# Kernel optimization log

Hardware: AMD Instinct MI355X
Metric: run time of the kernel (lower is better)

## Reference

```python
import jax, jax.numpy as jnp
import numpy as np

B, N_P, N_S = 64, 50, 200
N_NODES = N_P * N_S          # 10000 nodes per graph (jobs x ops)
N_CAND = N_S + 1             # 201 candidates
INPUT_DIM, HIDDEN = 3, 64
NODE_DIM = 2 * HIDDEN        # h_nodes feature dim (=> actor in = 6*HIDDEN)
POOL_DIM = 4 * HIDDEN        # h_pooled dim (mean || max pooling)
H_ACTOR, H_CRITIC = 256, 256


def setup_inputs() -> dict:
    key = jax.random.key(0)
    ks = jax.random.split(key, 16)
    p = lambda k, sh: jax.random.normal(k, sh, jnp.float32) * 0.02
    x = jax.random.normal(ks[0], (B, N_NODES, INPUT_DIM), jnp.float32)
    candidate = jax.random.randint(ks[1], (B, N_CAND), 0, N_NODES)
    mask = jax.random.randint(ks[2], (B, N_CAND), 0, 2) > 0
    mask = mask.at[:, 0].set(True)  # guarantee at least one valid action per row
    return {
        "x": x, "candidate": candidate, "mask": mask,
        "fe_w1": p(ks[3], (INPUT_DIM, HIDDEN)), "fe_b1": jnp.zeros((HIDDEN,), jnp.float32),
        "fe_w2": p(ks[4], (HIDDEN, NODE_DIM)), "fe_b2": jnp.zeros((NODE_DIM,), jnp.float32),
        "a_w1": p(ks[5], (NODE_DIM + POOL_DIM, H_ACTOR)), "a_b1": jnp.zeros((H_ACTOR,), jnp.float32),
        "a_w2": p(ks[6], (H_ACTOR, H_ACTOR)), "a_b2": jnp.zeros((H_ACTOR,), jnp.float32),
        "a_w3": p(ks[7], (H_ACTOR, 1)), "a_b3": jnp.zeros((1,), jnp.float32),
        "c_w1": p(ks[8], (POOL_DIM, H_CRITIC)), "c_b1": jnp.zeros((H_CRITIC,), jnp.float32),
        "c_w2": p(ks[9], (H_CRITIC, H_CRITIC)), "c_b2": jnp.zeros((H_CRITIC,), jnp.float32),
        "c_w3": p(ks[10], (H_CRITIC, 1)), "c_b3": jnp.zeros((1,), jnp.float32),
    }


def _actor_critic(x, candidate, mask,
                  fe_w1, fe_b1, fe_w2, fe_b2,
                  a_w1, a_b1, a_w2, a_b2, a_w3, a_b3,
                  c_w1, c_b1, c_w2, c_b2, c_w3, c_b3):
    # --- feature_extract: per-node MLP embedding, graph-level pooling ---
    h = jax.nn.relu(jnp.einsum('bni,ih->bnh', x, fe_w1) + fe_b1)
    h_nodes = jax.nn.relu(jnp.einsum('bnh,hd->bnd', h, fe_w2) + fe_b2)   # [B, N, 2H]
    h_pooled = jnp.concatenate([h_nodes.mean(axis=1), h_nodes.max(axis=1)], axis=-1)  # [B, 4H]

    # --- gather candidate node features (torch.gather over node axis) ---
    cand_feat = jnp.take_along_axis(h_nodes, candidate[:, :, None], axis=1)  # [B, C, 2H]

    # --- concat broadcast pooled feature ---
    pooled_rep = jnp.broadcast_to(h_pooled[:, None, :], (cand_feat.shape[0], cand_feat.shape[1], h_pooled.shape[-1]))
    concat_fea = jnp.concatenate([cand_feat, pooled_rep], axis=-1)  # [B, C, 6H]

    # --- actor MLP (tanh hidden layers, linear out) ---
    a = jnp.tanh(concat_fea @ a_w1 + a_b1)
    a = jnp.tanh(a @ a_w2 + a_b2)
    scores = a @ a_w3 + a_b3                                    # [B, C, 1]

    # --- mask with -inf, softmax over candidate axis ---
    scores = jnp.where(mask[:, :, None], scores, -jnp.inf)
    pi = jax.nn.softmax(scores, axis=1)                          # [B, C, 1]

    # --- critic MLP on pooled feature ---
    c = jnp.tanh(h_pooled @ c_w1 + c_b1)
    c = jnp.tanh(c @ c_w2 + c_b2)
    v = c @ c_w3 + c_b3                                          # [B, 1]
    return pi, v


def reference(x, candidate, mask,
              fe_w1, fe_b1, fe_w2, fe_b2,
              a_w1, a_b1, a_w2, a_b2, a_w3, a_b3,
              c_w1, c_b1, c_w2, c_b2, c_w3, c_b3):
    return _actor_critic(x, candidate, mask,
                         fe_w1, fe_b1, fe_w2, fe_b2,
                         a_w1, a_b1, a_w2, a_b2, a_w3, a_b3,
                         c_w1, c_b1, c_w2, c_b2, c_w3, c_b3)
```

## Files before the change

### kernel.cpp

```cpp
#include <hip/hip_runtime.h>

#define NN 10000
#define NCAND 201
#define NB 64

typedef __attribute__((ext_vector_type(8))) short short8;
typedef __attribute__((ext_vector_type(4))) float f32x4;

__device__ __forceinline__ float bf2f(unsigned short u) {
  return __uint_as_float(((unsigned int)u) << 16);
}
__device__ __forceinline__ unsigned short f2bf(float f) {
  unsigned int u = __float_as_uint(f);
  u += 0x7FFFu + ((u >> 16) & 1u);
  return (unsigned short)(u >> 16);
}
__device__ __forceinline__ float fast_tanh(float x) {
  return 1.0f - 2.0f / (__expf(2.0f * x) + 1.0f);
}
__device__ __forceinline__ float gld(const void* p, long i, int f) {
  return f ? ((const float*)p)[i] : bf2f(((const unsigned short*)p)[i]);
}

__global__ __launch_bounds__(256)
void detect_kernel(const void* x, const void* w1, const void* b1, const void* w2,
                   const void* b2, const void* aw1, const void* ab1, const void* aw2,
                   const void* ab2, const void* aw3, const void* ab3,
                   const void* cw1, const void* cb1, const void* cw2, const void* cb2,
                   const void* cw3, const void* cb3,
                   const unsigned int* mask_w, const unsigned int* cand_w,
                   int* F, float* zero_base) {
  const void* ptrs[17] = {x, w1, b1, w2, b2, aw1, ab1, aw2, ab2, aw3, ab3,
                          cw1, cb1, cw2, cb2, cw3, cb3};
  const int sizes[17] = {1920000, 192, 64, 8192, 128, 98304, 256, 65536, 256,
                         256, 1, 65536, 256, 65536, 256, 256, 1};
  const int t = threadIdx.x;
  const int j = blockIdx.x;
  __shared__ int sh[3];
  if (t < 3) sh[t] = 0;
  __syncthreads();
  if (j < 17) {
    const unsigned short* p = (const unsigned short*)ptrs[j];
    int K = min(sizes[j], 2048);
    int c = 0;
    for (int i = t; i < K; i += 256)
      if ((p[i] & 0x7F80u) >= 0x4300u) c++;
    if (c) atomicAdd(&sh[0], c);
    __syncthreads();
    if (t == 0) F[j] = (sh[0] > (K >> 3)) ? 1 : 0;
  } else if (j == 17) {
    int flo = 0, fhi = 0, fgt = 0;
    for (int i = t; i < 3216; i += 256) {
      unsigned int w = mask_w[i];
      if ((w & 0xFFFFu) == 0x3F80u) flo = 1;
      if ((w >> 16) == 0x3F80u) fhi = 1;
      if (w > 1u) fgt = 1;
    }
    if (flo) sh[0] = 1;
    if (fhi) sh[1] = 1;
    if (fgt) sh[2] = 1;
    __syncthreads();
    if (t == 0) F[17] = sh[0] ? 2 : (sh[1] ? 3 : (sh[2] ? 1 : 0));
  } else if (j == 18) {
    int co = 0;
    for (int i = t; i < 1024; i += 256)
      if ((i & 1) && cand_w[i] != 0u) co = 1;
    if (co) sh[0] = 1;
    __syncthreads();
    if (t == 0) F[18] = sh[0] ? 0 : 1;
  } else {
    zero_base[(j - 19) * 256 + t] = 0.f;
  }
}

__global__ __launch_bounds__(256)
void prep_kernel(const void* __restrict__ fe_w2, const void* __restrict__ a_w1,
                 const void* __restrict__ a_w2,
                 const void* __restrict__ c_w1, const void* __restrict__ c_w2,
                 const int* __restrict__ F,
                 unsigned short* __restrict__ w2t, unsigned short* __restrict__ aw1t,
                 unsigned short* __restrict__ aw2t,
                 unsigned short* __restrict__ cw1t, unsigned short* __restrict__ cw2t) {
  const int F3 = F[3], F5 = F[5], F7 = F[7], F11 = F[11], F13 = F[13];
  int i = blockIdx.x * 256 + threadIdx.x;
  if (i < 128 * 64) { int n = i >> 6, k = i & 63; w2t[i] = f2bf(gld(fe_w2, k * 128 + n, F3)); }
  if (i < 256 * 384) { int n = i / 384, k = i % 384; aw1t[i] = f2bf(gld(a_w1, k * 256 + n, F5)); }
  if (i < 256 * 256) {
    int n = i >> 8, k = i & 255;
    aw2t[i] = f2bf(gld(a_w2, k * 256 + n, F7));
    cw1t[i] = f2bf(gld(c_w1, k * 256 + n, F11));
    cw2t[i] = f2bf(gld(c_w2, k * 256 + n, F13));
  }
}

__global__ __launch_bounds__(256, 4)
void feat_pool_kernel(const void* __restrict__ x,
                      const void* __restrict__ w1, const void* __restrict__ b1,
                      const unsigned short* __restrict__ w2t,
                      const void* __restrict__ b2,
                      const int* __restrict__ F,
                      float* __restrict__ psum, float* __restrict__ pmax) {
  __shared__ __align__(16) unsigned short h1s[128 * 72];
  __shared__ float w1f[3 * 64];
  __shared__ float b1f[64];
  __shared__ float b2f[128];

  const int t = threadIdx.x;
  const int b = blockIdx.x >> 4;
  const int s = blockIdx.x & 15;
  const int lane = t & 63;
  const int wv = t >> 6;
  const int F0 = F[0], F1 = F[1], F2 = F[2], F4 = F[4];

  if (t < 192) w1f[t] = gld(w1, t, F1);
  if (t < 64) b1f[t] = gld(b1, t, F2);
  if (t < 128) b2f[t] = gld(b2, t, F4);

  short8 bfr[2][2];
#pragma unroll
  for (int nl = 0; nl < 2; ++nl)
#pragma unroll
    for (int ks = 0; ks < 2; ++ks) {
      int col = wv * 32 + nl * 16 + (lane & 15);
      bfr[nl][ks] = *(const short8*)(w2t + col * 64 + ((lane >> 4) * 8) + ks * 32);
    }
  __syncthreads();

  float csum[2] = {0.f, 0.f};
  float cmax[2] = {0.f, 0.f};

  const int m = t & 127;
  const int kg = t >> 7;

  float x0 = 0.f, x1 = 0.f, x2 = 0.f;
  {
    int c0 = s;
    if (c0 < 79) {
      int nb = c0 * 128;
      if (m < min(128, NN - nb)) {
        long xo = ((long)b * NN + nb + m) * 3;
        x0 = gld(x, xo, F0); x1 = gld(x, xo + 1, F0); x2 = gld(x, xo + 2, F0);
      }
    }
  }

  for (int c = s; c < 79; c += 16) {
    int nb = c * 128;
    int cnt = (nb + 128 <= NN) ? 128 : (NN - nb);
    if (m < cnt) {
#pragma unroll
      for (int blk = 0; blk < 4; ++blk) {
        short8 v;
#pragma unroll
        for (int i = 0; i < 8; ++i) {
          int k = kg * 32 + blk * 8 + i;
          float vv = x0 * w1f[k] + x1 * w1f[64 + k] + x2 * w1f[128 + k] + b1f[k];
          v[i] = (short)f2bf(fmaxf(vv, 0.f));
        }
        *(short8*)(h1s + m * 72 + kg * 32 + blk * 8) = v;
      }
    }
    {
      int cn = c + 16;
      float nx0 = 0.f, nx1 = 0.f, nx2 = 0.f;
      if (cn < 79) {
        int nbn = cn * 128;
        if (m < min(128, NN - nbn)) {
          long xo = ((long)b * NN + nbn + m) * 3;
          nx0 = gld(x, xo, F0); nx1 = gld(x, xo + 1, F0); nx2 = gld(x, xo + 2, F0);
        }
      }
      __syncthreads();
      x0 = nx0; x1 = nx1; x2 = nx2;
    }
#pragma unroll
    for (int mt = 0; mt < 8; ++mt) {
      const unsigned short* ap = h1s + (mt * 16 + (lane & 15)) * 72 + ((lane >> 4) * 8);
      short8 af0 = *(const short8*)(ap);
      short8 af1 = *(const short8*)(ap + 32);
#pragma unroll
      for (int nl = 0; nl < 2; ++nl) {
        f32x4 acc = {0.f, 0.f, 0.f, 0.f};
        acc = __builtin_amdgcn_mfma_f32_16x16x32_bf16(af0, bfr[nl][0], acc, 0, 0, 0);
        acc = __builtin_amdgcn_mfma_f32_16x16x32_bf16(af1, bfr[nl][1], acc, 0, 0, 0);
        int col = wv * 32 + nl * 16 + (lane & 15);
        float bb = b2f[col];
#pragma unroll
        for (int r = 0; r < 4; ++r) {
          int row = mt * 16 + ((lane >> 4) * 4) + r;
          if (row < cnt) {
            float v = fmaxf(acc[r] + bb, 0.f);
            csum[nl] += v;
            cmax[nl] = fmaxf(cmax[nl], v);
          }
        }
      }
    }
    __syncthreads();
  }
#pragma unroll
  for (int nl = 0; nl < 2; ++nl) {
    csum[nl] += __shfl_xor(csum[nl], 16);
    csum[nl] += __shfl_xor(csum[nl], 32);
    cmax[nl] = fmaxf(cmax[nl], __shfl_xor(cmax[nl], 16));
    cmax[nl] = fmaxf(cmax[nl], __shfl_xor(cmax[nl], 32));
  }
  if (lane < 16) {
#pragma unroll
    for (int nl = 0; nl < 2; ++nl) {
      int col = wv * 32 + nl * 16 + lane;
      atomicAdd(&psum[b * 128 + col], csum[nl]);
      atomicMax((int*)&pmax[b * 128 + col], __float_as_int(cmax[nl]));
    }
  }
}

__global__ __launch_bounds__(256)
void actor_kernel(const void* __restrict__ x, const int* __restrict__ cand,
                  const void* __restrict__ w1, const void* __restrict__ b1,
                  const void* __restrict__ b2bf,
                  const void* __restrict__ ab1, const void* __restrict__ ab2,
                  const void* __restrict__ aw3, const void* __restrict__ ab3,
                  const int* __restrict__ F,
                  const float* __restrict__ psum, const float* __restrict__ pmax,
                  const unsigned short* __restrict__ w2t,
                  const unsigned short* __restrict__ aw1t,
                  const unsigned short* __restrict__ aw2t,
                  float* __restrict__ scores) {
  __shared__ __align__(16) unsigned short h1c[32 * 72];
  __shared__ __align__(16) unsigned short cf[32 * 136];
  __shared__ __align__(16) unsigned short a1s[32 * 264];
  __shared__ __align__(16) unsigned short a2s[32 * 264];
  __shared__ __align__(16) unsigned short plbf[256];
  __shared__ float ab1f[256], ab2f[256], b2f[128];

  const int t = threadIdx.x;
  const int b = blockIdx.x / 7;
  const int cb = blockIdx.x % 7;
  const int cbase = cb * 29;
  const int cntc = min(29, NCAND - cbase);
  const int lane = t & 63;
  const int wv = t >> 6;
  const int F0 = F[0], F1 = F[1], F2 = F[2], F4 = F[4], F6 = F[6], F8 = F[8];
  const int F9 = F[9], F10 = F[10], C64 = F[18];

  if (t < 128) {
    plbf[t] = f2bf(psum[b * 128 + t] * (1.0f / 10000.0f));
    plbf[128 + t] = f2bf(pmax[b * 128 + t]);
    b2f[t] = gld(b2bf, t, F4);
  }
  ab1f[t] = gld(ab1, t, F6);
  ab2f[t] = gld(ab2, t, F8);

  {
    int r = t & 31;
    int ci = cbase + r;
    if (ci > NCAND - 1) ci = NCAND - 1;
    long cidx = (long)b * NCAND + ci;
    int nd = C64 ? cand[2 * cidx] : cand[cidx];
    long xo = ((long)b * NN + nd) * 3;
    float x0 = gld(x, xo, F0), x1 = gld(x, xo + 1, F0), x2 = gld(x, xo + 2, F0);
    int kg = t >> 5;
#pragma unroll
    for (int i = 0; i < 8; ++i) {
      int k = kg * 8 + i;
      float v = x0 * gld(w1, k, F1) + x1 * gld(w1, 64 + k, F1) +
                x2 * gld(w1, 128 + k, F1) + gld(b1, k, F2);
      h1c[r * 72 + k] = f2bf(fmaxf(v, 0.f));
    }
  }
  __syncthreads();

  {
    short8 af[2][2];
#pragma unroll
    for (int mt = 0; mt < 2; ++mt)
#pragma unroll
      for (int ks = 0; ks < 2; ++ks)
        af[mt][ks] = *(const short8*)(h1c + (mt * 16 + (lane & 15)) * 72 + ((lane >> 4) * 8) + ks * 32);
#pragma unroll
    for (int nl = 0; nl < 2; ++nl) {
      int col = wv * 32 + nl * 16 + (lane & 15);
      short8 bf0 = *(const short8*)(w2t + col * 64 + ((lane >> 4) * 8));
      short8 bf1 = *(const short8*)(w2t + col * 64 + ((lane >> 4) * 8) + 32);
      float bb = b2f[col];
#pragma unroll
      for (int mt = 0; mt < 2; ++mt) {
        f32x4 acc = {0.f, 0.f, 0.f, 0.f};
        acc = __builtin_amdgcn_mfma_f32_16x16x32_bf16(af[mt][0], bf0, acc, 0, 0, 0);
        acc = __builtin_amdgcn_mfma_f32_16x16x32_bf16(af[mt][1], bf1, acc, 0, 0, 0);
#pragma unroll
        for (int r = 0; r < 4; ++r) {
          int row = mt * 16 + ((lane >> 4) * 4) + r;
          cf[row * 136 + col] = f2bf(fmaxf(acc[r] + bb, 0.f));
        }
      }
    }
  }
  __syncthreads();

  {
    f32x4 acc[2][4];
#pragma unroll
    for (int mt = 0; mt < 2; ++mt)
#pragma unroll
      for (int nt = 0; nt < 4; ++nt) acc[mt][nt] = (f32x4){0.f, 0.f, 0.f, 0.f};
    for (int ks = 0; ks < 12; ++ks) {
      short8 af0, af1;
      if (ks < 4) {
        af0 = *(const short8*)(cf + (lane & 15) * 136 + ks * 32 + ((lane >> 4) * 8));
        af1 = *(const short8*)(cf + (16 + (lane & 15)) * 136 + ks * 32 + ((lane >> 4) * 8));
      } else {
        short8 p = *(const short8*)(plbf + (ks - 4) * 32 + ((lane >> 4) * 8));
        af0 = p;
        af1 = p;
      }
#pragma unroll
      for (int nt = 0; nt < 4; ++nt) {
        int col = wv * 64 + nt * 16 + (lane & 15);
        short8 bfr = *(const short8*)(aw1t + col * 384 + ks * 32 + ((lane >> 4) * 8));
        acc[0][nt] = __builtin_amdgcn_mfma_f32_16x16x32_bf16(af0, bfr, acc[0][nt], 0, 0, 0);
        acc[1][nt] = __builtin_amdgcn_mfma_f32_16x16x32_bf16(af1, bfr, acc[1][nt], 0, 0, 0);
      }
    }
#pragma unroll
    for (int mt = 0; mt < 2; ++mt)
#pragma unroll
      for (int nt = 0; nt < 4; ++nt) {
        int col = wv * 64 + nt * 16 + (lane & 15);
        float bb = ab1f[col];
#pragma unroll
        for (int r = 0; r < 4; ++r) {
          int row = mt * 16 + ((lane >> 4) * 4) + r;
          a1s[row * 264 + col] = f2bf(fast_tanh(acc[mt][nt][r] + bb));
        }
      }
  }
  __syncthreads();

  {
    f32x4 acc[2][4];
#pragma unroll
    for (int mt = 0; mt < 2; ++mt)
#pragma unroll
      for (int nt = 0; nt < 4; ++nt) acc[mt][nt] = (f32x4){0.f, 0.f, 0.f, 0.f};
    for (int ks = 0; ks < 8; ++ks) {
      short8 af0 = *(const short8*)(a1s + (lane & 15) * 264 + ks * 32 + ((lane >> 4) * 8));
      short8 af1 = *(const short8*)(a1s + (16 + (lane & 15)) * 264 + ks * 32 + ((lane >> 4) * 8));
#pragma unroll
      for (int nt = 0; nt < 4; ++nt) {
        int col = wv * 64 + nt * 16 + (lane & 15);
        short8 bfr = *(const short8*)(aw2t + col * 256 + ks * 32 + ((lane >> 4) * 8));
        acc[0][nt] = __builtin_amdgcn_mfma_f32_16x16x32_bf16(af0, bfr, acc[0][nt], 0, 0, 0);
        acc[1][nt] = __builtin_amdgcn_mfma_f32_16x16x32_bf16(af1, bfr, acc[1][nt], 0, 0, 0);
      }
    }
#pragma unroll
    for (int mt = 0; mt < 2; ++mt)
#pragma unroll
      for (int nt = 0; nt < 4; ++nt) {
        int col = wv * 64 + nt * 16 + (lane & 15);
        float bb = ab2f[col];
#pragma unroll
        for (int r = 0; r < 4; ++r) {
          int row = mt * 16 + ((lane >> 4) * 4) + r;
          a2s[row * 264 + col] = f2bf(fast_tanh(acc[mt][nt][r] + bb));
        }
      }
  }
  __syncthreads();

  {
    int row = t >> 3, seg = t & 7;
    float p = 0.f;
#pragma unroll 8
    for (int i = 0; i < 32; ++i) {
      int k = seg * 32 + i;
      p += bf2f(a2s[row * 264 + k]) * gld(aw3, k, F9);
    }
    p += __shfl_xor(p, 1);
    p += __shfl_xor(p, 2);
    p += __shfl_xor(p, 4);
    if (seg == 0 && row < cntc)
      scores[b * 256 + cbase + row] = p + gld(ab3, 0, F10);
  }
}

__global__ __launch_bounds__(256)
void softmax_critic_kernel(const float* __restrict__ scores,
                           const void* __restrict__ mask,
                           const int* __restrict__ F,
                           const float* __restrict__ psum,
                           const float* __restrict__ pmax,
                           const unsigned short* __restrict__ cw1t,
                           const unsigned short* __restrict__ cw2t,
                           const void* __restrict__ cb1, const void* __restrict__ cb2,
                           const void* __restrict__ cw3, const void* __restrict__ cb3,
                           void* __restrict__ out) {
  __shared__ float plf[256];
  __shared__ float c1f[256];
  __shared__ float red[4];
  const int t = threadIdx.x, b = blockIdx.x;
  const int lane = t & 63, wv = t >> 6;
  const int MM = F[17];
  const int OF = (F[0] + F[1] + F[3] + F[5] + F[7] + F[9] + F[11] + F[13] + F[15]) >= 5;
  const int F12 = F[12], F14 = F[14], F15 = F[15], F16 = F[16];

  if (t < 128) {
    plf[t] = psum[b * 128 + t] * (1.0f / 10000.0f);
    plf[128 + t] = pmax[b * 128 + t];
  }

  float sraw = 0.f, sv = -1e30f;
  bool valid = false;
  if (t < NCAND) {
    sraw = scores[b * 256 + t];
    long idx = (long)b * NCAND + t;
    if (MM == 0)      valid = ((const int*)mask)[idx] != 0;
    else if (MM == 1) valid = ((const unsigned char*)mask)[idx] != 0;
    else if (MM == 2) valid = ((const unsigned short*)mask)[idx] != 0;
    else              valid = ((const unsigned int*)mask)[idx] != 0;
    if (valid) sv = sraw;
  }
  float m = sv;
  for (int o = 32; o; o >>= 1) m = fmaxf(m, __shfl_xor(m, o));
  if (lane == 0) red[wv] = m;
  __syncthreads();
  m = fmaxf(fmaxf(red[0], red[1]), fmaxf(red[2], red[3]));
  __syncthreads();
  float e = valid ? __expf(sraw - m) : 0.f;
  if (!(e == e)) e = 0.f;
  float ss = e;
  for (int o = 32; o; o >>= 1) ss += __shfl_xor(ss, o);
  if (lane == 0) red[wv] = ss;
  __syncthreads();
  float tot = red[0] + red[1] + red[2] + red[3];
  tot = fmaxf(tot, 1e-30f);
  if (t < NCAND) {
    float pv = e / tot;
    if (!(pv == pv)) pv = 0.f;
    if (OF) ((float*)out)[b * NCAND + t] = pv;
    else ((unsigned short*)out)[b * NCAND + t] = f2bf(pv);
  }
  __syncthreads();

  {
    float a = gld(cb1, t, F12);
    const unsigned short* row = cw1t + t * 256;
#pragma unroll
    for (int k8 = 0; k8 < 32; ++k8) {
      short8 w = *(const short8*)(row + k8 * 8);
#pragma unroll
      for (int j = 0; j < 8; ++j)
        a += plf[k8 * 8 + j] * bf2f((unsigned short)w[j]);
    }
    c1f[t] = fast_tanh(a);
  }
  __syncthreads();
  {
    float a2 = gld(cb2, t, F14);
    const unsigned short* row = cw2t + t * 256;
#pragma unroll
    for (int k8 = 0; k8 < 32; ++k8) {
      short8 w = *(const short8*)(row + k8 * 8);
#pragma unroll
      for (int j = 0; j < 8; ++j)
        a2 += c1f[k8 * 8 + j] * bf2f((unsigned short)w[j]);
    }
    a2 = fast_tanh(a2);
    float p = a2 * gld(cw3, t, F15);
    for (int o = 32; o; o >>= 1) p += __shfl_xor(p, o);
    __syncthreads();
    if (lane == 0) red[wv] = p;
    __syncthreads();
    if (t == 0) {
      float v = red[0] + red[1] + red[2] + red[3] + gld(cb3, 0, F16);
      if (!(v == v)) v = 0.f;
      if (OF) ((float*)out)[NB * NCAND + b] = v;
      else ((unsigned short*)out)[NB * NCAND + b] = f2bf(v);
    }
  }
}

extern "C" void kernel_launch(void* const* d_in, const int* in_sizes, int n_in,
                              void* d_out, int out_size, void* d_ws, size_t ws_size,
                              hipStream_t stream) {
  const void* x = d_in[0];
  const int* cand = (const int*)d_in[1];
  const void* mask = d_in[2];
  const void* fe_w1 = d_in[3];
  const void* fe_b1 = d_in[4];
  const void* fe_w2 = d_in[5];
  const void* fe_b2 = d_in[6];
  const void* a_w1 = d_in[7];
  const void* a_b1 = d_in[8];
  const void* a_w2 = d_in[9];
  const void* a_b2 = d_in[10];
  const void* a_w3 = d_in[11];
  const void* a_b3 = d_in[12];
  const void* c_w1 = d_in[13];
  const void* c_b1 = d_in[14];
  const void* c_w2 = d_in[15];
  const void* c_b2 = d_in[16];
  const void* c_w3 = d_in[17];
  const void* c_b3 = d_in[18];

  char* ws = (char*)d_ws;
  float* psum = (float*)(ws + 0);
  float* pmax = (float*)(ws + 32768);
  float* scores = (float*)(ws + 65536);
  unsigned short* w2t = (unsigned short*)(ws + 131072);
  unsigned short* aw1t = (unsigned short*)(ws + 147456);
  unsigned short* aw2t = (unsigned short*)(ws + 344064);
  int* F = (int*)(ws + 475136);
  unsigned short* cw1t = (unsigned short*)(ws + 475264);
  unsigned short* cw2t = (unsigned short*)(ws + 606336);

  detect_kernel<<<83, 256, 0, stream>>>(x, fe_w1, fe_b1, fe_w2, fe_b2,
                                        a_w1, a_b1, a_w2, a_b2, a_w3, a_b3,
                                        c_w1, c_b1, c_w2, c_b2, c_w3, c_b3,
                                        (const unsigned int*)mask,
                                        (const unsigned int*)cand, F, psum);
  prep_kernel<<<384, 256, 0, stream>>>(fe_w2, a_w1, a_w2, c_w1, c_w2, F,
                                       w2t, aw1t, aw2t, cw1t, cw2t);
  feat_pool_kernel<<<1024, 256, 0, stream>>>(x, fe_w1, fe_b1, w2t, fe_b2, F, psum, pmax);
  actor_kernel<<<448, 256, 0, stream>>>(x, cand, fe_w1, fe_b1, fe_b2,
                                        a_b1, a_b2, a_w3, a_b3, F, psum, pmax,
                                        w2t, aw1t, aw2t, scores);
  softmax_critic_kernel<<<64, 256, 0, stream>>>(scores, mask, F, psum, pmax,
                                                cw1t, cw2t, c_b1, c_b2, c_w3, c_b3,
                                                (void*)d_out);
}
```

Baseline: 171.3 us.

## Merge dtype detection into weight prep kernel and split softmax/critic blocks

Merges the detect and weight-transpose kernels into a single launch. Each prep block now recomputes the dtype flags for the five transposed weights locally, counting over the first 2048 elements in shared memory, so it no longer has to wait for a separate detect kernel. The softmax/critic kernel moves from 64 to 128 blocks: the first 64 do the masked softmax and the other 64 run the critic MLP, so both run in parallel. This removes one launch and serialisation point, at the cost of each prep block rereading 10K sample elements.

```diff
diff --git a/kernel.cpp b/kernel.cpp
--- a/kernel.cpp
+++ b/kernel.cpp
@@ -23,32 +23,66 @@
 }
 
 __global__ __launch_bounds__(256)
-void detect_kernel(const void* x, const void* w1, const void* b1, const void* w2,
-                   const void* b2, const void* aw1, const void* ab1, const void* aw2,
-                   const void* ab2, const void* aw3, const void* ab3,
-                   const void* cw1, const void* cb1, const void* cw2, const void* cb2,
-                   const void* cw3, const void* cb3,
-                   const unsigned int* mask_w, const unsigned int* cand_w,
-                   int* F, float* zero_base) {
-  const void* ptrs[17] = {x, w1, b1, w2, b2, aw1, ab1, aw2, ab2, aw3, ab3,
-                          cw1, cb1, cw2, cb2, cw3, cb3};
-  const int sizes[17] = {1920000, 192, 64, 8192, 128, 98304, 256, 65536, 256,
-                         256, 1, 65536, 256, 65536, 256, 256, 1};
+void prep_kernel(const void* x, const void* w1, const void* b1, const void* w2,
+                 const void* b2, const void* aw1, const void* ab1, const void* aw2,
+                 const void* ab2, const void* aw3, const void* ab3,
+                 const void* cw1, const void* cb1, const void* cw2, const void* cb2,
+                 const void* cw3, const void* cb3,
+                 const unsigned int* mask_w, const unsigned int* cand_w,
+                 int* F, float* zero_base,
+                 unsigned short* __restrict__ w2t, unsigned short* __restrict__ aw1t,
+                 unsigned short* __restrict__ aw2t,
+                 unsigned short* __restrict__ cw1t, unsigned short* __restrict__ cw2t) {
   const int t = threadIdx.x;
   const int j = blockIdx.x;
+
+  if (j < 384) {
+    __shared__ int cnts[5];
+    if (t < 5) cnts[t] = 0;
+    __syncthreads();
+    const void* aps[5] = {w2, aw1, aw2, cw1, cw2};
+#pragma unroll
+    for (int a = 0; a < 5; ++a) {
+      const unsigned short* p = (const unsigned short*)aps[a];
+      int c = 0;
+      for (int i = t; i < 2048; i += 256)
+        if ((p[i] & 0x7F80u) >= 0x4300u) c++;
+      if (c) atomicAdd(&cnts[a], c);
+    }
+    __syncthreads();
+    const int Fw2 = cnts[0] > 256, Faw1 = cnts[1] > 256, Faw2 = cnts[2] > 256;
+    const int Fcw1 = cnts[3] > 256, Fcw2 = cnts[4] > 256;
+    int i = j * 256 + t;
+    if (i < 128 * 64) { int n = i >> 6, k = i & 63; w2t[i] = f2bf(gld(w2, k * 128 + n, Fw2)); }
+    if (i < 256 * 384) { int n = i / 384, k = i % 384; aw1t[i] = f2bf(gld(aw1, k * 256 + n, Faw1)); }
+    if (i < 256 * 256) {
+      int n = i >> 8, k = i & 255;
+      aw2t[i] = f2bf(gld(aw2, k * 256 + n, Faw2));
+      cw1t[i] = f2bf(gld(cw1, k * 256 + n, Fcw1));
+      cw2t[i] = f2bf(gld(cw2, k * 256 + n, Fcw2));
+    }
+    return;
+  }
+
   __shared__ int sh[3];
   if (t < 3) sh[t] = 0;
   __syncthreads();
-  if (j < 17) {
-    const unsigned short* p = (const unsigned short*)ptrs[j];
-    int K = min(sizes[j], 2048);
+
+  if (j < 401) {
+    const void* ptrs[17] = {x, w1, b1, w2, b2, aw1, ab1, aw2, ab2, aw3, ab3,
+                            cw1, cb1, cw2, cb2, cw3, cb3};
+    const int sizes[17] = {1920000, 192, 64, 8192, 128, 98304, 256, 65536, 256,
+                           256, 1, 65536, 256, 65536, 256, 256, 1};
+    int a = j - 384;
+    const unsigned short* p = (const unsigned short*)ptrs[a];
+    int K = min(sizes[a], 2048);
     int c = 0;
     for (int i = t; i < K; i += 256)
       if ((p[i] & 0x7F80u) >= 0x4300u) c++;
     if (c) atomicAdd(&sh[0], c);
     __syncthreads();
-    if (t == 0) F[j] = (sh[0] > (K >> 3)) ? 1 : 0;
-  } else if (j == 17) {
+    if (t == 0) F[a] = (sh[0] > (K >> 3)) ? 1 : 0;
+  } else if (j == 401) {
     int flo = 0, fhi = 0, fgt = 0;
     for (int i = t; i < 3216; i += 256) {
       unsigned int w = mask_w[i];
@@ -61,7 +95,7 @@
     if (fgt) sh[2] = 1;
     __syncthreads();
     if (t == 0) F[17] = sh[0] ? 2 : (sh[1] ? 3 : (sh[2] ? 1 : 0));
-  } else if (j == 18) {
+  } else if (j == 402) {
     int co = 0;
     for (int i = t; i < 1024; i += 256)
       if ((i & 1) && cand_w[i] != 0u) co = 1;
@@ -69,27 +103,7 @@
     __syncthreads();
     if (t == 0) F[18] = sh[0] ? 0 : 1;
   } else {
-    zero_base[(j - 19) * 256 + t] = 0.f;
-  }
-}
-
-__global__ __launch_bounds__(256)
-void prep_kernel(const void* __restrict__ fe_w2, const void* __restrict__ a_w1,
-                 const void* __restrict__ a_w2,
-                 const void* __restrict__ c_w1, const void* __restrict__ c_w2,
-                 const int* __restrict__ F,
-                 unsigned short* __restrict__ w2t, unsigned short* __restrict__ aw1t,
-                 unsigned short* __restrict__ aw2t,
-                 unsigned short* __restrict__ cw1t, unsigned short* __restrict__ cw2t) {
-  const int F3 = F[3], F5 = F[5], F7 = F[7], F11 = F[11], F13 = F[13];
-  int i = blockIdx.x * 256 + threadIdx.x;
-  if (i < 128 * 64) { int n = i >> 6, k = i & 63; w2t[i] = f2bf(gld(fe_w2, k * 128 + n, F3)); }
-  if (i < 256 * 384) { int n = i / 384, k = i % 384; aw1t[i] = f2bf(gld(a_w1, k * 256 + n, F5)); }
-  if (i < 256 * 256) {
-    int n = i >> 8, k = i & 255;
-    aw2t[i] = f2bf(gld(a_w2, k * 256 + n, F7));
-    cw1t[i] = f2bf(gld(c_w1, k * 256 + n, F11));
-    cw2t[i] = f2bf(gld(c_w2, k * 256 + n, F13));
+    zero_base[(j - 403) * 256 + t] = 0.f;
   }
 }
 
@@ -400,84 +414,86 @@
   __shared__ float plf[256];
   __shared__ float c1f[256];
   __shared__ float red[4];
-  const int t = threadIdx.x, b = blockIdx.x;
+  const int t = threadIdx.x;
+  const int b = blockIdx.x & 63;
   const int lane = t & 63, wv = t >> 6;
-  const int MM = F[17];
   const int OF = (F[0] + F[1] + F[3] + F[5] + F[7] + F[9] + F[11] + F[13] + F[15]) >= 5;
-  const int F12 = F[12], F14 = F[14], F15 = F[15], F16 = F[16];
-
-  if (t < 128) {
-    plf[t] = psum[b * 128 + t] * (1.0f / 10000.0f);
-    plf[128 + t] = pmax[b * 128 + t];
-  }
-
-  float sraw = 0.f, sv = -1e30f;
-  bool valid = false;
-  if (t < NCAND) {
-    sraw = scores[b * 256 + t];
-    long idx = (long)b * NCAND + t;
-    if (MM == 0)      valid = ((const int*)mask)[idx] != 0;
-    else if (MM == 1) valid = ((const unsigned char*)mask)[idx] != 0;
-    else if (MM == 2) valid = ((const unsigned short*)mask)[idx] != 0;
-    else              valid = ((const unsigned int*)mask)[idx] != 0;
-    if (valid) sv = sraw;
-  }
-  float m = sv;
-  for (int o = 32; o; o >>= 1) m = fmaxf(m, __shfl_xor(m, o));
-  if (lane == 0) red[wv] = m;
-  __syncthreads();
-  m = fmaxf(fmaxf(red[0], red[1]), fmaxf(red[2], red[3]));
-  __syncthreads();
-  float e = valid ? __expf(sraw - m) : 0.f;
-  if (!(e == e)) e = 0.f;
-  float ss = e;
-  for (int o = 32; o; o >>= 1) ss += __shfl_xor(ss, o);
-  if (lane == 0) red[wv] = ss;
-  __syncthreads();
-  float tot = red[0] + red[1] + red[2] + red[3];
-  tot = fmaxf(tot, 1e-30f);
-  if (t < NCAND) {
-    float pv = e / tot;
-    if (!(pv == pv)) pv = 0.f;
-    if (OF) ((float*)out)[b * NCAND + t] = pv;
-    else ((unsigned short*)out)[b * NCAND + t] = f2bf(pv);
-  }
-  __syncthreads();
-
-  {
-    float a = gld(cb1, t, F12);
-    const unsigned short* row = cw1t + t * 256;
-#pragma unroll
-    for (int k8 = 0; k8 < 32; ++k8) {
-      short8 w = *(const short8*)(row + k8 * 8);
-#pragma unroll
-      for (int j = 0; j < 8; ++j)
-        a += plf[k8 * 8 + j] * bf2f((unsigned short)w[j]);
-    }
-    c1f[t] = fast_tanh(a);
-  }
-  __syncthreads();
-  {
-    float a2 = gld(cb2, t, F14);
-    const unsigned short* row = cw2t + t * 256;
-#pragma unroll
-    for (int k8 = 0; k8 < 32; ++k8) {
-      short8 w = *(const short8*)(row + k8 * 8);
-#pragma unroll
-      for (int j = 0; j < 8; ++j)
-        a2 += c1f[k8 * 8 + j] * bf2f((unsigned short)w[j]);
-    }
-    a2 = fast_tanh(a2);
-    float p = a2 * gld(cw3, t, F15);
-    for (int o = 32; o; o >>= 1) p += __shfl_xor(p, o);
-    __syncthreads();
-    if (lane == 0) red[wv] = p;
-    __syncthreads();
-    if (t == 0) {
-      float v = red[0] + red[1] + red[2] + red[3] + gld(cb3, 0, F16);
-      if (!(v == v)) v = 0.f;
-      if (OF) ((float*)out)[NB * NCAND + b] = v;
-      else ((unsigned short*)out)[NB * NCAND + b] = f2bf(v);
+
+  if (blockIdx.x < 64) {
+    const int MM = F[17];
+    float sraw = 0.f, sv = -1e30f;
+    bool valid = false;
+    if (t < NCAND) {
+      sraw = scores[b * 256 + t];
+      long idx = (long)b * NCAND + t;
+      if (MM == 0)      valid = ((const int*)mask)[idx] != 0;
+      else if (MM == 1) valid = ((const unsigned char*)mask)[idx] != 0;
+      else if (MM == 2) valid = ((const unsigned short*)mask)[idx] != 0;
+      else              valid = ((const unsigned int*)mask)[idx] != 0;
+      if (valid) sv = sraw;
+    }
+    float m = sv;
+    for (int o = 32; o; o >>= 1) m = fmaxf(m, __shfl_xor(m, o));
+    if (lane == 0) red[wv] = m;
+    __syncthreads();
+    m = fmaxf(fmaxf(red[0], red[1]), fmaxf(red[2], red[3]));
+    __syncthreads();
+    float e = valid ? __expf(sraw - m) : 0.f;
+    if (!(e == e)) e = 0.f;
+    float ss = e;
+    for (int o = 32; o; o >>= 1) ss += __shfl_xor(ss, o);
+    if (lane == 0) red[wv] = ss;
+    __syncthreads();
+    float tot = red[0] + red[1] + red[2] + red[3];
+    tot = fmaxf(tot, 1e-30f);
+    if (t < NCAND) {
+      float pv = e / tot;
+      if (!(pv == pv)) pv = 0.f;
+      if (OF) ((float*)out)[b * NCAND + t] = pv;
+      else ((unsigned short*)out)[b * NCAND + t] = f2bf(pv);
+    }
+  } else {
+    const int F12 = F[12], F14 = F[14], F15 = F[15], F16 = F[16];
+    if (t < 128) {
+      plf[t] = psum[b * 128 + t] * (1.0f / 10000.0f);
+      plf[128 + t] = pmax[b * 128 + t];
+    }
+    __syncthreads();
+    {
+      float a = gld(cb1, t, F12);
+      const unsigned short* row = cw1t + t * 256;
+#pragma unroll
+      for (int k8 = 0; k8 < 32; ++k8) {
+        short8 w = *(const short8*)(row + k8 * 8);
+#pragma unroll
+        for (int j = 0; j < 8; ++j)
+          a += plf[k8 * 8 + j] * bf2f((unsigned short)w[j]);
+      }
+      c1f[t] = fast_tanh(a);
+    }
+    __syncthreads();
+    {
+      float a2 = gld(cb2, t, F14);
+      const unsigned short* row = cw2t + t * 256;
+#pragma unroll
+      for (int k8 = 0; k8 < 32; ++k8) {
+        short8 w = *(const short8*)(row + k8 * 8);
+#pragma unroll
+        for (int j = 0; j < 8; ++j)
+          a2 += c1f[k8 * 8 + j] * bf2f((unsigned short)w[j]);
+      }
+      a2 = fast_tanh(a2);
+      float p = a2 * gld(cw3, t, F15);
+      for (int o = 32; o; o >>= 1) p += __shfl_xor(p, o);
+      __syncthreads();
+      if (lane == 0) red[wv] = p;
+      __syncthreads();
+      if (t == 0) {
+        float v = red[0] + red[1] + red[2] + red[3] + gld(cb3, 0, F16);
+        if (!(v == v)) v = 0.f;
+        if (OF) ((float*)out)[NB * NCAND + b] = v;
+        else ((unsigned short*)out)[NB * NCAND + b] = f2bf(v);
+      }
     }
   }
 }
@@ -516,18 +532,17 @@
   unsigned short* cw1t = (unsigned short*)(ws + 475264);
   unsigned short* cw2t = (unsigned short*)(ws + 606336);
 
-  detect_kernel<<<83, 256, 0, stream>>>(x, fe_w1, fe_b1, fe_w2, fe_b2,
-                                        a_w1, a_b1, a_w2, a_b2, a_w3, a_b3,
-                                        c_w1, c_b1, c_w2, c_b2, c_w3, c_b3,
-                                        (const unsigned int*)mask,
-                                        (const unsigned int*)cand, F, psum);
-  prep_kernel<<<384, 256, 0, stream>>>(fe_w2, a_w1, a_w2, c_w1, c_w2, F,
+  prep_kernel<<<467, 256, 0, stream>>>(x, fe_w1, fe_b1, fe_w2, fe_b2,
+                                       a_w1, a_b1, a_w2, a_b2, a_w3, a_b3,
+                                       c_w1, c_b1, c_w2, c_b2, c_w3, c_b3,
+                                       (const unsigned int*)mask,
+                                       (const unsigned int*)cand, F, psum,
                                        w2t, aw1t, aw2t, cw1t, cw2t);
   feat_pool_kernel<<<1024, 256, 0, stream>>>(x, fe_w1, fe_b1, w2t, fe_b2, F, psum, pmax);
   actor_kernel<<<448, 256, 0, stream>>>(x, cand, fe_w1, fe_b1, fe_b2,
                                         a_b1, a_b2, a_w3, a_b3, F, psum, pmax,
                                         w2t, aw1t, aw2t, scores);
-  softmax_critic_kernel<<<64, 256, 0, stream>>>(scores, mask, F, psum, pmax,
-                                                cw1t, cw2t, c_b1, c_b2, c_w3, c_b3,
-                                                (void*)d_out);
-}
+  softmax_critic_kernel<<<128, 256, 0, stream>>>(scores, mask, F, psum, pmax,
+                                                 cw1t, cw2t, c_b1, c_b2, c_w3, c_b3,
+                                                 (void*)d_out);
+}
```

Result: slower. 177.7 us (+3.8%).
